# Performance work log

Measured on AMD Instinct MI355X. Metric: run time of the kernel, lower is better.

The kernel has to match this reference:

```python
import jax, jax.numpy as jnp
import numpy as np

B, S, E, H = 2, 1024, 4096, 16
D = E // H          # head_dim = 256
RD = 64             # rotary_dim
# Quantization scales (alpha of the int8 GEMM epilogues)
A_QKV = 1.2e-4      # W8A8B8O8 q/k/v projection output scale
A_QK = 2e-4         # BMM_S8T_S8N_F32T alpha (= q_scale * k_scale)
A_PV = 1.0 / 127.0  # BMM_S8T_S8N_S8T alpha (probs quantized by *127)
A_O = 0.01          # W8A8BFP32OFP32 out_proj alpha


def setup_inputs() -> dict:
    key = jax.random.key(0)
    ks = jax.random.split(key, 9)
    ri = lambda k, shp: jax.random.randint(k, shp, -127, 128).astype(jnp.float32)
    return {
        "hidden_states": ri(ks[0], (B, S, E)),   # int8-valued activations
        "Wq": ri(ks[1], (E, E)),
        "Wk": ri(ks[2], (E, E)),
        "Wv": ri(ks[3], (E, E)),
        "Wo": ri(ks[4], (E, E)),
        "bq": ri(ks[5], (E,)),
        "bk": ri(ks[6], (E,)),
        "bv": ri(ks[7], (E,)),
        "bo": jax.random.normal(ks[8], (E,), dtype=jnp.float32) * 0.02,  # fp32 bias
    }


def _linear_i8(x, W, b, alpha):
    # W8A8B8O8Linear: int8 GEMM, scaled, +int8 bias, round+saturate to int8
    y = alpha * (x @ W.T) + b
    return jnp.clip(jnp.round(y), -128, 127)


def _rotate_every_two(x):
    x1 = x[..., ::2]
    x2 = x[..., 1::2]
    return jnp.stack((-x2, x1), axis=-1).reshape(x.shape)


def _apply_rotary(x, sin, cos):
    # duplicate_interleave == repeat each column twice; broadcast over [B, S, H, rd]
    sin = jnp.repeat(sin, 2, axis=-1)[None, :, None, :]
    cos = jnp.repeat(cos, 2, axis=-1)[None, :, None, :]
    r = x * cos + _rotate_every_two(x) * sin
    # torch: clamp(-128,127).to(int8) -> truncate toward zero
    return jnp.trunc(jnp.clip(r, -128.0, 127.0))


def reference(hidden_states, Wq, Wk, Wv, Wo, bq, bk, bv, bo):
    q = _linear_i8(hidden_states, Wq, bq, A_QKV).reshape(B, S, H, D)
    k = _linear_i8(hidden_states, Wk, bk, A_QKV).reshape(B, S, H, D)
    v = _linear_i8(hidden_states, Wv, bv, A_QKV).reshape(B, S, H, D)
    v = v.transpose(0, 2, 1, 3)  # [B, H, S, D]

    # fixed_pos_embedding over rotary_dim
    inv_freq = 1.0 / (10000.0 ** (jnp.arange(0, RD, 2, dtype=jnp.float32) / RD))
    t = jnp.arange(S, dtype=jnp.float32)
    sinusoid = t[:, None] * inv_freq[None, :]   # [S, RD/2]
    sin, cos = jnp.sin(sinusoid), jnp.cos(sinusoid)

    q = jnp.concatenate([_apply_rotary(q[..., :RD], sin, cos), q[..., RD:]], axis=-1)
    k = jnp.concatenate([_apply_rotary(k[..., :RD], sin, cos), k[..., RD:]], axis=-1)
    q = q.transpose(0, 2, 1, 3)  # [B, H, S, D]
    k = k.transpose(0, 2, 1, 3)

    w = A_QK * jnp.einsum('bhqd,bhkd->bhqk', q, k)
    causal = jnp.tril(jnp.ones((S, S), dtype=bool))[None, None]
    w = jnp.where(causal, w, jnp.finfo(jnp.float32).min)
    w = w / jnp.sqrt(jnp.float32(D))  # scale_attn = sqrt(head_dim)
    p = jnp.round(jax.nn.softmax(w, axis=-1) * 127.0)  # int8-valued probs

    # pv_bmm: int8 probs x int8 values -> scaled, round+saturate to int8
    o = jnp.clip(jnp.round(A_PV * jnp.einsum('bhqk,bhkd->bhqd', p, v)), -128, 127)
    o = o.transpose(0, 2, 1, 3).reshape(B, S, E)  # merge heads

    # out_proj: W8A8BFP32OFP32 -> fp32 output
    return A_O * (o @ Wo.T) + bo
```

## Files before the change

### kernel.cpp

```cpp
#include <hip/hip_runtime.h>
#include <hip/hip_bf16.h>

typedef int int32x4 __attribute__((ext_vector_type(4)));
typedef signed char i8;

#define B_ 2
#define S_ 1024
#define E_ 4096
#define H_ 16
#define D_ 256

#define MFMA_I8(a, b, c) __builtin_amdgcn_mfma_i32_16x16x64_i8((a), (b), (c), 0, 0, 0)

__device__ __forceinline__ int32x4 ld16(const void* p) {
    return *reinterpret_cast<const int32x4*>(p);
}

__device__ __forceinline__ void gload16(const void* g, void* l) {
    __builtin_amdgcn_global_load_lds(
        (const __attribute__((address_space(1))) void*)g,
        (__attribute__((address_space(3))) void*)l, 16, 0, 0);
}

#define WAIT_VM3()  asm volatile("s_waitcnt vmcnt(3)" ::: "memory")
#define WAIT_VM0()  asm volatile("s_waitcnt vmcnt(0)" ::: "memory")
#define WAIT_LGKM0() do { asm volatile("s_waitcnt lgkmcnt(0)" ::: "memory"); \
                          __builtin_amdgcn_sched_barrier(0); } while (0)

__device__ __forceinline__ int pack4(float4 f) {
    union { int w; i8 b[4]; } u;
    u.b[0] = (i8)f.x; u.b[1] = (i8)f.y; u.b[2] = (i8)f.z; u.b[3] = (i8)f.w;
    return u.w;
}

__global__ void k_f32_to_i8(const float* __restrict__ src, i8* __restrict__ dst, int n4) {
    int i = blockIdx.x * blockDim.x + threadIdx.x;
    if (i >= n4) return;
    reinterpret_cast<int*>(dst)[i] = pack4(reinterpret_cast<const float4*>(src)[i]);
}

__global__ void k_w_to_i8(const float* __restrict__ w0, const float* __restrict__ w1,
                          const float* __restrict__ w2, const float* __restrict__ w3,
                          i8* __restrict__ d0, i8* __restrict__ d1,
                          i8* __restrict__ d2, i8* __restrict__ d3, int n4) {
    int i = blockIdx.x * blockDim.x + threadIdx.x;
    if (i >= n4) return;
    const float* src = (blockIdx.y == 0) ? w0 : (blockIdx.y == 1) ? w1 : (blockIdx.y == 2) ? w2 : w3;
    i8* dst = (blockIdx.y == 0) ? d0 : (blockIdx.y == 1) ? d1 : (blockIdx.y == 2) ? d2 : d3;
    reinterpret_cast<int*>(dst)[i] = pack4(reinterpret_cast<const float4*>(src)[i]);
}

__global__ void k_sincos(float* __restrict__ sin_t, float* __restrict__ cos_t) {
    int idx = blockIdx.x * blockDim.x + threadIdx.x;
    if (idx >= S_ * 32) return;
    int s = idx >> 5, i = idx & 31;
    float ex = (float)(2 * i) / 64.0f;
    float invf = 1.0f / powf(10000.0f, ex);
    float arg = (float)s * invf;
    sin_t[idx] = (float)sin((double)arg);
    cos_t[idx] = (float)cos((double)arg);
}

template<bool OUT_I8>
__device__ __forceinline__ void gemm_core(
    const i8* __restrict__ X, const i8* __restrict__ W, const float* __restrict__ bias,
    void* __restrict__ out, float alpha, int M, int N, int K, i8* lds)
{
    const int nt = K >> 6;
    const int nwg = (M >> 8) * (N >> 7);
    const int q = nwg >> 3;
    const int lin = blockIdx.x;
    const int wg = (lin & 7) * q + (lin >> 3);
    const int nbm = M >> 8;
    const int m0 = (wg % nbm) * 256, n0 = (wg / nbm) * 128;

    const int tid = threadIdx.x, lane = tid & 63, wave = tid >> 6;
    const int wr = wave >> 1, wc = wave & 1, l4 = lane & 15, lh = lane >> 4;

    const int g4 = lh ^ ((l4 >> 1) & 3);
    const int aoff = (wr * 64 + l4) * 64 + g4 * 16;
    const int boff = 16384 + (wc * 64 + l4) * 64 + g4 * 16;

    const int srow = tid >> 2;
    const int sg = (tid & 3) ^ ((tid >> 3) & 3);
    const i8* Asrc = X + (size_t)(m0 + srow) * K + sg * 16;
    const i8* Bsrc = W + (size_t)(n0 + srow) * K + sg * 16;
    const size_t rstep = (size_t)128 * K;
    const int ldst = wave * 1024;

#define BUF(t_) (lds + ((t_) % 3) * 24576)
#define STAGE_A(t_) do { int kb_ = (t_) * 64; i8* lb_ = BUF(t_);             \
        gload16(Asrc + kb_,         lb_ + ldst);                             \
        gload16(Asrc + rstep + kb_, lb_ + 8192 + ldst); } while (0)
#define STAGE_B(t_) do { int kb_ = (t_) * 64; i8* lb_ = BUF(t_);             \
        gload16(Bsrc + kb_,         lb_ + 16384 + ldst); } while (0)

    int32x4 acc[4][4];
#pragma unroll
    for (int m = 0; m < 4; ++m)
#pragma unroll
        for (int n = 0; n < 4; ++n) acc[m][n] = int32x4{0, 0, 0, 0};

    STAGE_A(0); STAGE_B(0);
    STAGE_A(1); STAGE_B(1);

    for (int t = 0; t < nt; ++t) {
        const i8* Tb = BUF(t);
        if (t + 1 < nt) { WAIT_VM3(); } else { WAIT_VM0(); }
        __builtin_amdgcn_s_barrier();

        int32x4 a0, a1, a2, a3, b0, b1, b2, b3;
        a0 = ld16(Tb + aoff);        a1 = ld16(Tb + aoff + 1024);
        b0 = ld16(Tb + boff);        b1 = ld16(Tb + boff + 1024);
        b2 = ld16(Tb + boff + 2048); b3 = ld16(Tb + boff + 3072);
        if (t + 2 < nt) STAGE_A(t + 2);
        __builtin_amdgcn_s_barrier();
        WAIT_LGKM0();
        __builtin_amdgcn_s_setprio(1);
        acc[0][0] = MFMA_I8(a0, b0, acc[0][0]);
        acc[0][1] = MFMA_I8(a0, b1, acc[0][1]);
        acc[0][2] = MFMA_I8(a0, b2, acc[0][2]);
        acc[0][3] = MFMA_I8(a0, b3, acc[0][3]);
        acc[1][0] = MFMA_I8(a1, b0, acc[1][0]);
        acc[1][1] = MFMA_I8(a1, b1, acc[1][1]);
        acc[1][2] = MFMA_I8(a1, b2, acc[1][2]);
        acc[1][3] = MFMA_I8(a1, b3, acc[1][3]);
        __builtin_amdgcn_s_setprio(0);
        __builtin_amdgcn_s_barrier();

        a2 = ld16(Tb + aoff + 2048); a3 = ld16(Tb + aoff + 3072);
        if (t + 2 < nt) STAGE_B(t + 2);
        __builtin_amdgcn_s_barrier();
        WAIT_LGKM0();
        __builtin_amdgcn_s_setprio(1);
        acc[2][0] = MFMA_I8(a2, b0, acc[2][0]);
        acc[2][1] = MFMA_I8(a2, b1, acc[2][1]);
        acc[2][2] = MFMA_I8(a2, b2, acc[2][2]);
        acc[2][3] = MFMA_I8(a2, b3, acc[2][3]);
        acc[3][0] = MFMA_I8(a3, b0, acc[3][0]);
        acc[3][1] = MFMA_I8(a3, b1, acc[3][1]);
        acc[3][2] = MFMA_I8(a3, b2, acc[3][2]);
        acc[3][3] = MFMA_I8(a3, b3, acc[3][3]);
        __builtin_amdgcn_s_setprio(0);
    }
#undef BUF
#undef STAGE_A
#undef STAGE_B

#pragma unroll
    for (int m = 0; m < 4; ++m)
#pragma unroll
        for (int n = 0; n < 4; ++n)
#pragma unroll
            for (int r = 0; r < 4; ++r) {
                int grow = m0 + wr * 64 + m * 16 + lh * 4 + r;
                int gcol = n0 + wc * 64 + n * 16 + l4;
                float y = alpha * (float)acc[m][n][r] + bias[gcol];
                if (OUT_I8) {
                    float v = rintf(y);
                    v = fminf(fmaxf(v, -128.0f), 127.0f);
                    reinterpret_cast<i8*>(out)[(size_t)grow * N + gcol] = (i8)v;
                } else {
                    reinterpret_cast<float*>(out)[(size_t)grow * N + gcol] = y;
                }
            }
}

__global__ __launch_bounds__(512, 4) void k_gemm_qkv(
    const i8* __restrict__ X,
    const i8* __restrict__ w0, const i8* __restrict__ w1, const i8* __restrict__ w2,
    const float* __restrict__ b0, const float* __restrict__ b1, const float* __restrict__ b2,
    i8* __restrict__ o0, i8* __restrict__ o1, i8* __restrict__ o2,
    float alpha, int M, int N, int K)
{
    __shared__ __align__(16) i8 lds[3 * 24576];
    int z = blockIdx.z;
    const i8* W = (z == 0) ? w0 : (z == 1) ? w1 : w2;
    const float* bias = (z == 0) ? b0 : (z == 1) ? b1 : b2;
    i8* out = (z == 0) ? o0 : (z == 1) ? o1 : o2;
    gemm_core<true>(X, W, bias, out, alpha, M, N, K, lds);
}

__global__ __launch_bounds__(512, 4) void k_gemm_out(
    const i8* __restrict__ X, const i8* __restrict__ W, const float* __restrict__ bias,
    float* __restrict__ out, float alpha, int M, int N, int K)
{
    __shared__ __align__(16) i8 lds[3 * 24576];
    gemm_core<false>(X, W, bias, out, alpha, M, N, K, lds);
}

__global__ void k_rope(const i8* __restrict__ qin, const i8* __restrict__ kin,
                       i8* __restrict__ qout, i8* __restrict__ kout,
                       const float* __restrict__ sin_t, const float* __restrict__ cos_t)
{
    const i8* in = blockIdx.y ? kin : qin;
    i8* outp = blockIdx.y ? kout : qout;
    int row = blockIdx.x * 2 + (threadIdx.x >> 7);
    int i = threadIdx.x & 127;
    int b = row / (S_ * H_);
    int s = (row / H_) % S_;
    int h = row % H_;
    const i8* src = in + (size_t)row * D_ + i * 2;
    i8 x1 = src[0], x2 = src[1];
    i8 o1, o2;
    if (i < 32) {
        float c = cos_t[s * 32 + i], sn = sin_t[s * 32 + i];
        float f1 = (float)x1, f2 = (float)x2;
        float r0 = __fadd_rn(__fmul_rn(f1, c), __fmul_rn(-f2, sn));
        float r1 = __fadd_rn(__fmul_rn(f2, c), __fmul_rn(f1, sn));
        r0 = truncf(fminf(fmaxf(r0, -128.0f), 127.0f));
        r1 = truncf(fminf(fmaxf(r1, -128.0f), 127.0f));
        o1 = (i8)r0; o2 = (i8)r1;
    } else { o1 = x1; o2 = x2; }
    size_t ob = ((size_t)(b * H_ + h) * S_ + s) * D_ + i * 2;
    outp[ob] = o1; outp[ob + 1] = o2;
}

__global__ void k_vtrans(const i8* __restrict__ vin, i8* __restrict__ vout) {
    __shared__ int tile[64][17];
    int bh = blockIdx.z;
    int b = bh >> 4, h = bh & 15;
    int s0 = blockIdx.x * 64, d0 = blockIdx.y * 64;
    int t = threadIdx.x;
    {
        int sr = t >> 2, dq = (t & 3) * 16;
        int32x4 v = ld16(vin + ((size_t)(b * S_ + s0 + sr) * H_ + h) * D_ + d0 + dq);
#pragma unroll
        for (int j = 0; j < 4; ++j) tile[sr][dq / 4 + j] = v[j];
    }
    __syncthreads();
    {
        int dr = t >> 2, sq = (t & 3) * 16;
        union { int32x4 v; i8 b[16]; } u;
        const i8* tb = reinterpret_cast<const i8*>(tile);
#pragma unroll
        for (int j = 0; j < 16; ++j) u.b[j] = tb[(sq + j) * 68 + dr];
        *reinterpret_cast<int32x4*>(vout + ((size_t)bh * D_ + d0 + dr) * S_ + s0 + sq) = u.v;
    }
}

struct AttnShared {
    float slx[4][32];
    float r127[32];
    __align__(16) i8 plds[32][80];
};

__device__ __forceinline__ void attn_chunk(int qc, int bh, int tid,
    const i8* __restrict__ Qh, const i8* __restrict__ Kb, const i8* __restrict__ Vb,
    i8* __restrict__ O, AttnShared& sh)
{
    const float C2 = 1.25e-5f * 1.44269504088896f;
    const float APV = 1.0f / 127.0f;
    const int lane = tid & 63, wave = tid >> 6;
    const int l4 = lane & 15, lh = lane >> 4;
    const i8* Qb = Qh + (size_t)(qc * 32) * D_;
    const int nt = (qc * 32 + 31) / 64 + 1;

    int32x4 aq[2][4];
#pragma unroll
    for (int m = 0; m < 2; ++m)
#pragma unroll
        for (int kk = 0; kk < 4; ++kk)
            aq[m][kk] = ld16(Qb + (size_t)(m * 16 + l4) * D_ + kk * 64 + lh * 16);

    float sum_[2][4];
#pragma unroll
    for (int m = 0; m < 2; ++m)
#pragma unroll
        for (int r = 0; r < 4; ++r) sum_[m][r] = 0.0f;

    for (int kt = 0; kt < nt; ++kt) {
        int cb = kt * 64 + wave * 16;
        int32x4 acc0 = int32x4{0,0,0,0}, acc1 = int32x4{0,0,0,0};
#pragma unroll
        for (int kk = 0; kk < 4; ++kk) {
            int32x4 bf = ld16(Kb + (size_t)(cb + l4) * D_ + kk * 64 + lh * 16);
            acc0 = MFMA_I8(aq[0][kk], bf, acc0);
            acc1 = MFMA_I8(aq[1][kk], bf, acc1);
        }
        int gcol = cb + l4;
#pragma unroll
        for (int m = 0; m < 2; ++m) {
            int32x4 accm = m ? acc1 : acc0;
#pragma unroll
            for (int r = 0; r < 4; ++r) {
                int grow = qc * 32 + m * 16 + lh * 4 + r;
                float e = (gcol <= grow) ? exp2f((float)accm[r] * C2) : 0.0f;
                sum_[m][r] += e;
            }
        }
    }

#pragma unroll
    for (int m = 0; m < 2; ++m)
#pragma unroll
        for (int r = 0; r < 4; ++r) {
            float s = sum_[m][r];
            s += __shfl_xor(s, 1);
            s += __shfl_xor(s, 2);
            s += __shfl_xor(s, 4);
            s += __shfl_xor(s, 8);
            if (l4 == 0) sh.slx[wave][m * 16 + lh * 4 + r] = s;
        }
    __syncthreads();
    if (tid < 32)
        sh.r127[tid] = 127.0f /
            (sh.slx[0][tid] + sh.slx[1][tid] + sh.slx[2][tid] + sh.slx[3][tid]);
    __syncthreads();

    int32x4 oacc[2][4];
#pragma unroll
    for (int m = 0; m < 2; ++m)
#pragma unroll
        for (int n = 0; n < 4; ++n) oacc[m][n] = int32x4{0, 0, 0, 0};

    for (int kt = 0; kt < nt; ++kt) {
        int cb = kt * 64 + wave * 16;
        int32x4 acc0 = int32x4{0,0,0,0}, acc1 = int32x4{0,0,0,0};
#pragma unroll
        for (int kk = 0; kk < 4; ++kk) {
            int32x4 bf = ld16(Kb + (size_t)(cb + l4) * D_ + kk * 64 + lh * 16);
            acc0 = MFMA_I8(aq[0][kk], bf, acc0);
            acc1 = MFMA_I8(aq[1][kk], bf, acc1);
        }
        int gcol = cb + l4;
        i8 pv[2][4];
#pragma unroll
        for (int m = 0; m < 2; ++m) {
            int32x4 accm = m ? acc1 : acc0;
#pragma unroll
            for (int r = 0; r < 4; ++r) {
                int rowi = m * 16 + lh * 4 + r;
                int grow = qc * 32 + rowi;
                float e = (gcol <= grow) ? exp2f((float)accm[r] * C2) : 0.0f;
                pv[m][r] = (i8)(int)rintf(e * sh.r127[rowi]);
            }
        }
        __syncthreads();
#pragma unroll
        for (int m = 0; m < 2; ++m)
#pragma unroll
            for (int r = 0; r < 4; ++r)
                sh.plds[m * 16 + lh * 4 + r][wave * 16 + l4] = pv[m][r];
        __syncthreads();
        int32x4 a0 = ld16(&sh.plds[l4][lh * 16]);
        int32x4 a1 = ld16(&sh.plds[16 + l4][lh * 16]);
#pragma unroll
        for (int n = 0; n < 4; ++n) {
            int32x4 bf = ld16(Vb + (size_t)(wave * 64 + n * 16 + l4) * S_ + kt * 64 + lh * 16);
            oacc[0][n] = MFMA_I8(a0, bf, oacc[0][n]);
            oacc[1][n] = MFMA_I8(a1, bf, oacc[1][n]);
        }
    }

    int b = bh >> 4, h = bh & 15;
#pragma unroll
    for (int m = 0; m < 2; ++m)
#pragma unroll
        for (int r = 0; r < 4; ++r) {
            int s = qc * 32 + m * 16 + lh * 4 + r;
#pragma unroll
            for (int n = 0; n < 4; ++n) {
                float o = rintf(APV * (float)oacc[m][n][r]);
                o = fminf(fmaxf(o, -128.0f), 127.0f);
                O[((size_t)(b * S_ + s) * H_ + h) * D_ + wave * 64 + n * 16 + l4] = (i8)o;
            }
        }
}

__global__ __launch_bounds__(256) void k_attn(const i8* __restrict__ Q, const i8* __restrict__ K,
                                              const i8* __restrict__ V, i8* __restrict__ O)
{
    __shared__ AttnShared sh;
    int bh = blockIdx.x;
    int p = blockIdx.y;
    int tid = threadIdx.x;
    const i8* Qh = Q + (size_t)bh * S_ * D_;
    const i8* Kb = K + (size_t)bh * S_ * D_;
    const i8* Vb = V + (size_t)bh * D_ * S_;
    attn_chunk((S_ / 32 - 1) - p, bh, tid, Qh, Kb, Vb, O, sh);
    attn_chunk(p, bh, tid, Qh, Kb, Vb, O, sh);
}

extern "C" void kernel_launch(void* const* d_in, const int* in_sizes, int n_in,
                              void* d_out, int out_size, void* d_ws, size_t ws_size,
                              hipStream_t stream) {
    const float* hs = (const float*)d_in[0];
    const float* Wq = (const float*)d_in[1];
    const float* Wk = (const float*)d_in[2];
    const float* Wv = (const float*)d_in[3];
    const float* Wo = (const float*)d_in[4];
    const float* bq = (const float*)d_in[5];
    const float* bk = (const float*)d_in[6];
    const float* bv = (const float*)d_in[7];
    const float* bo = (const float*)d_in[8];
    float* out = (float*)d_out;

    size_t off = 0;
    char* wsb = (char*)d_ws;
    auto carve = [&](size_t bytes) { char* p = wsb + off; off += (bytes + 255) & ~(size_t)255; return p; };
    const size_t ME = (size_t)B_ * S_ * E_;
    const size_t EE = (size_t)E_ * E_;
    i8* x8  = (i8*)carve(ME);
    i8* wq8 = (i8*)carve(EE);
    i8* wk8 = (i8*)carve(EE);
    i8* wv8 = (i8*)carve(EE);
    i8* wo8 = (i8*)carve(EE);
    i8* q8  = (i8*)carve(ME);
    i8* k8  = (i8*)carve(ME);
    i8* v8  = (i8*)carve(ME);
    i8* qr  = (i8*)carve(ME);
    i8* kr  = (i8*)carve(ME);
    i8* vt  = (i8*)carve(ME);
    i8* o8  = (i8*)carve(ME);
    float* sin_t = (float*)carve((size_t)S_ * 32 * 4);
    float* cos_t = (float*)carve((size_t)S_ * 32 * 4);

    int n4_me = (int)(ME / 4), n4_ee = (int)(EE / 4);
    k_f32_to_i8<<<(n4_me + 255) / 256, 256, 0, stream>>>(hs, x8, n4_me);
    k_w_to_i8<<<dim3((n4_ee + 255) / 256, 4), 256, 0, stream>>>(
        Wq, Wk, Wv, Wo, wq8, wk8, wv8, wo8, n4_ee);
    k_sincos<<<(S_ * 32 + 255) / 256, 256, 0, stream>>>(sin_t, cos_t);

    const int M = B_ * S_, N = E_, Kd = E_;
    const int nwg = (M / 256) * (N / 128);
    k_gemm_qkv<<<dim3(nwg, 1, 3), 512, 0, stream>>>(
        x8, wq8, wk8, wv8, bq, bk, bv, q8, k8, v8, 0.00012f, M, N, Kd);

    k_rope<<<dim3((B_ * S_ * H_) / 2, 2), 256, 0, stream>>>(q8, k8, qr, kr, sin_t, cos_t);
    k_vtrans<<<dim3(S_ / 64, D_ / 64, B_ * H_), 256, 0, stream>>>(v8, vt);
    k_attn<<<dim3(B_ * H_, S_ / 64), 256, 0, stream>>>(qr, kr, vt, o8);

    k_gemm_out<<<nwg, 512, 0, stream>>>(o8, wo8, bo, out, 0.01f, M, N, Kd);
}
```

Before: 301.1 us.

## Use 4-wave GEMM with 128x64 per-wave tiles and one-chunk attention blocks

The int8 GEMM core moves from 8 waves of 64x64 to 4 waves of 128x64, doubling accumulators per wave and raising B-fragment reuse. Staging is regrouped into two phases of three loads each, with the vmcnt wait raised to match. Launch bounds drop to 256 threads with 2 blocks per CU. Attention now launches one 32-query chunk per block with heaviest chunks first, replacing the paired-chunk balancing. The larger per-wave tile raises register pressure and the attention grid relies on the hardware scheduler for balance.

```diff
diff --git a/kernel.cpp b/kernel.cpp
--- a/kernel.cpp
+++ b/kernel.cpp
@@ -22,7 +22,7 @@
         (__attribute__((address_space(3))) void*)l, 16, 0, 0);
 }
 
-#define WAIT_VM3()  asm volatile("s_waitcnt vmcnt(3)" ::: "memory")
+#define WAIT_VM6()  asm volatile("s_waitcnt vmcnt(6)" ::: "memory")
 #define WAIT_VM0()  asm volatile("s_waitcnt vmcnt(0)" ::: "memory")
 #define WAIT_LGKM0() do { asm volatile("s_waitcnt lgkmcnt(0)" ::: "memory"); \
                           __builtin_amdgcn_sched_barrier(0); } while (0)
@@ -78,42 +78,46 @@
     const int wr = wave >> 1, wc = wave & 1, l4 = lane & 15, lh = lane >> 4;
 
     const int g4 = lh ^ ((l4 >> 1) & 3);
-    const int aoff = (wr * 64 + l4) * 64 + g4 * 16;
+    const int aoff = (wr * 128 + l4) * 64 + g4 * 16;
     const int boff = 16384 + (wc * 64 + l4) * 64 + g4 * 16;
 
     const int srow = tid >> 2;
     const int sg = (tid & 3) ^ ((tid >> 3) & 3);
     const i8* Asrc = X + (size_t)(m0 + srow) * K + sg * 16;
     const i8* Bsrc = W + (size_t)(n0 + srow) * K + sg * 16;
-    const size_t rstep = (size_t)128 * K;
+    const size_t rstep = (size_t)64 * K;
     const int ldst = wave * 1024;
 
 #define BUF(t_) (lds + ((t_) % 3) * 24576)
-#define STAGE_A(t_) do { int kb_ = (t_) * 64; i8* lb_ = BUF(t_);             \
-        gload16(Asrc + kb_,         lb_ + ldst);                             \
-        gload16(Asrc + rstep + kb_, lb_ + 8192 + ldst); } while (0)
-#define STAGE_B(t_) do { int kb_ = (t_) * 64; i8* lb_ = BUF(t_);             \
-        gload16(Bsrc + kb_,         lb_ + 16384 + ldst); } while (0)
-
-    int32x4 acc[4][4];
-#pragma unroll
-    for (int m = 0; m < 4; ++m)
+#define STAGE_P1(t_) do { int kb_ = (t_) * 64; i8* lb_ = BUF(t_);            \
+        gload16(Asrc + kb_,               lb_ + ldst);                       \
+        gload16(Asrc + rstep + kb_,       lb_ + 4096 + ldst);                \
+        gload16(Bsrc + kb_,               lb_ + 16384 + ldst); } while (0)
+#define STAGE_P2(t_) do { int kb_ = (t_) * 64; i8* lb_ = BUF(t_);            \
+        gload16(Asrc + 2 * rstep + kb_,   lb_ + 8192 + ldst);                \
+        gload16(Asrc + 3 * rstep + kb_,   lb_ + 12288 + ldst);               \
+        gload16(Bsrc + rstep + kb_,       lb_ + 20480 + ldst); } while (0)
+
+    int32x4 acc[8][4];
+#pragma unroll
+    for (int m = 0; m < 8; ++m)
 #pragma unroll
         for (int n = 0; n < 4; ++n) acc[m][n] = int32x4{0, 0, 0, 0};
 
-    STAGE_A(0); STAGE_B(0);
-    STAGE_A(1); STAGE_B(1);
+    STAGE_P1(0); STAGE_P2(0);
+    STAGE_P1(1); STAGE_P2(1);
 
     for (int t = 0; t < nt; ++t) {
         const i8* Tb = BUF(t);
-        if (t + 1 < nt) { WAIT_VM3(); } else { WAIT_VM0(); }
+        if (t + 1 < nt) { WAIT_VM6(); } else { WAIT_VM0(); }
         __builtin_amdgcn_s_barrier();
 
         int32x4 a0, a1, a2, a3, b0, b1, b2, b3;
         a0 = ld16(Tb + aoff);        a1 = ld16(Tb + aoff + 1024);
+        a2 = ld16(Tb + aoff + 2048); a3 = ld16(Tb + aoff + 3072);
         b0 = ld16(Tb + boff);        b1 = ld16(Tb + boff + 1024);
         b2 = ld16(Tb + boff + 2048); b3 = ld16(Tb + boff + 3072);
-        if (t + 2 < nt) STAGE_A(t + 2);
+        if (t + 2 < nt) STAGE_P1(t + 2);
         __builtin_amdgcn_s_barrier();
         WAIT_LGKM0();
         __builtin_amdgcn_s_setprio(1);
@@ -125,14 +129,6 @@
         acc[1][1] = MFMA_I8(a1, b1, acc[1][1]);
         acc[1][2] = MFMA_I8(a1, b2, acc[1][2]);
         acc[1][3] = MFMA_I8(a1, b3, acc[1][3]);
-        __builtin_amdgcn_s_setprio(0);
-        __builtin_amdgcn_s_barrier();
-
-        a2 = ld16(Tb + aoff + 2048); a3 = ld16(Tb + aoff + 3072);
-        if (t + 2 < nt) STAGE_B(t + 2);
-        __builtin_amdgcn_s_barrier();
-        WAIT_LGKM0();
-        __builtin_amdgcn_s_setprio(1);
         acc[2][0] = MFMA_I8(a2, b0, acc[2][0]);
         acc[2][1] = MFMA_I8(a2, b1, acc[2][1]);
         acc[2][2] = MFMA_I8(a2, b2, acc[2][2]);
@@ -142,18 +138,43 @@
         acc[3][2] = MFMA_I8(a3, b2, acc[3][2]);
         acc[3][3] = MFMA_I8(a3, b3, acc[3][3]);
         __builtin_amdgcn_s_setprio(0);
+        __builtin_amdgcn_s_barrier();
+
+        a0 = ld16(Tb + aoff + 4096); a1 = ld16(Tb + aoff + 5120);
+        a2 = ld16(Tb + aoff + 6144); a3 = ld16(Tb + aoff + 7168);
+        if (t + 2 < nt) STAGE_P2(t + 2);
+        __builtin_amdgcn_s_barrier();
+        WAIT_LGKM0();
+        __builtin_amdgcn_s_setprio(1);
+        acc[4][0] = MFMA_I8(a0, b0, acc[4][0]);
+        acc[4][1] = MFMA_I8(a0, b1, acc[4][1]);
+        acc[4][2] = MFMA_I8(a0, b2, acc[4][2]);
+        acc[4][3] = MFMA_I8(a0, b3, acc[4][3]);
+        acc[5][0] = MFMA_I8(a1, b0, acc[5][0]);
+        acc[5][1] = MFMA_I8(a1, b1, acc[5][1]);
+        acc[5][2] = MFMA_I8(a1, b2, acc[5][2]);
+        acc[5][3] = MFMA_I8(a1, b3, acc[5][3]);
+        acc[6][0] = MFMA_I8(a2, b0, acc[6][0]);
+        acc[6][1] = MFMA_I8(a2, b1, acc[6][1]);
+        acc[6][2] = MFMA_I8(a2, b2, acc[6][2]);
+        acc[6][3] = MFMA_I8(a2, b3, acc[6][3]);
+        acc[7][0] = MFMA_I8(a3, b0, acc[7][0]);
+        acc[7][1] = MFMA_I8(a3, b1, acc[7][1]);
+        acc[7][2] = MFMA_I8(a3, b2, acc[7][2]);
+        acc[7][3] = MFMA_I8(a3, b3, acc[7][3]);
+        __builtin_amdgcn_s_setprio(0);
     }
 #undef BUF
-#undef STAGE_A
-#undef STAGE_B
-
-#pragma unroll
-    for (int m = 0; m < 4; ++m)
+#undef STAGE_P1
+#undef STAGE_P2
+
+#pragma unroll
+    for (int m = 0; m < 8; ++m)
 #pragma unroll
         for (int n = 0; n < 4; ++n)
 #pragma unroll
             for (int r = 0; r < 4; ++r) {
-                int grow = m0 + wr * 64 + m * 16 + lh * 4 + r;
+                int grow = m0 + wr * 128 + m * 16 + lh * 4 + r;
                 int gcol = n0 + wc * 64 + n * 16 + l4;
                 float y = alpha * (float)acc[m][n][r] + bias[gcol];
                 if (OUT_I8) {
@@ -166,7 +187,7 @@
             }
 }
 
-__global__ __launch_bounds__(512, 4) void k_gemm_qkv(
+__global__ __launch_bounds__(256, 2) void k_gemm_qkv(
     const i8* __restrict__ X,
     const i8* __restrict__ w0, const i8* __restrict__ w1, const i8* __restrict__ w2,
     const float* __restrict__ b0, const float* __restrict__ b1, const float* __restrict__ b2,
@@ -181,7 +202,7 @@
     gemm_core<true>(X, W, bias, out, alpha, M, N, K, lds);
 }
 
-__global__ __launch_bounds__(512, 4) void k_gemm_out(
+__global__ __launch_bounds__(256, 2) void k_gemm_out(
     const i8* __restrict__ X, const i8* __restrict__ W, const float* __restrict__ bias,
     float* __restrict__ out, float alpha, int M, int N, int K)
 {
@@ -372,14 +393,13 @@
                                               const i8* __restrict__ V, i8* __restrict__ O)
 {
     __shared__ AttnShared sh;
-    int bh = blockIdx.x;
-    int p = blockIdx.y;
+    int bh = blockIdx.y;
+    int qc = (S_ / 32 - 1) - blockIdx.x;
     int tid = threadIdx.x;
     const i8* Qh = Q + (size_t)bh * S_ * D_;
     const i8* Kb = K + (size_t)bh * S_ * D_;
     const i8* Vb = V + (size_t)bh * D_ * S_;
-    attn_chunk((S_ / 32 - 1) - p, bh, tid, Qh, Kb, Vb, O, sh);
-    attn_chunk(p, bh, tid, Qh, Kb, Vb, O, sh);
+    attn_chunk(qc, bh, tid, Qh, Kb, Vb, O, sh);
 }
 
 extern "C" void kernel_launch(void* const* d_in, const int* in_sizes, int n_in,
@@ -424,12 +444,12 @@
 
     const int M = B_ * S_, N = E_, Kd = E_;
     const int nwg = (M / 256) * (N / 128);
-    k_gemm_qkv<<<dim3(nwg, 1, 3), 512, 0, stream>>>(
+    k_gemm_qkv<<<dim3(nwg, 1, 3), 256, 0, stream>>>(
         x8, wq8, wk8, wv8, bq, bk, bv, q8, k8, v8, 0.00012f, M, N, Kd);
 
     k_rope<<<dim3((B_ * S_ * H_) / 2, 2), 256, 0, stream>>>(q8, k8, qr, kr, sin_t, cos_t);
     k_vtrans<<<dim3(S_ / 64, D_ / 64, B_ * H_), 256, 0, stream>>>(v8, vt);
-    k_attn<<<dim3(B_ * H_, S_ / 64), 256, 0, stream>>>(qr, kr, vt, o8);
-
-    k_gemm_out<<<nwg, 512, 0, stream>>>(o8, wo8, bo, out, 0.01f, M, N, Kd);
-}
+    k_attn<<<dim3(S_ / 32, B_ * H_), 256, 0, stream>>>(qr, kr, vt, o8);
+
+    k_gemm_out<<<nwg, 256, 0, stream>>>(o8, wo8, bo, out, 0.01f, M, N, Kd);
+}
```

After: 350.0 us. +16.2%, slower.
